# Kernel optimization log

Measured on AMD Instinct MI355X. Metric: run time of the kernel, lower is better.

The kernel has to match this reference:

```python
import jax, jax.numpy as jnp
import numpy as np

N_NODES = 50000


def _gcn_norm(edge_index, num_nodes):
    # Add self-loops (PyG GCNConv default) and compute symmetric norm.
    loops = jnp.arange(num_nodes, dtype=edge_index.dtype)
    src = jnp.concatenate([edge_index[0], loops])
    dst = jnp.concatenate([edge_index[1], loops])
    ones = jnp.ones(src.shape[0], dtype=jnp.float32)
    deg = jax.ops.segment_sum(ones, dst, num_segments=num_nodes)
    deg_inv_sqrt = jnp.where(deg > 0, jax.lax.rsqrt(jnp.maximum(deg, 1.0)), 0.0)
    norm = deg_inv_sqrt[src] * deg_inv_sqrt[dst]  # [E + N]
    return src, dst, norm


def _gcn_conv(x, src, dst, norm, W, b, num_nodes):
    xw = x @ W                               # [N, out]
    msg = xw[src] * norm[:, None]            # gather + scale  [E+N, out]
    out = jax.ops.segment_sum(msg, dst, num_segments=num_nodes)  # scatter-add
    return out + b


def setup_inputs() -> dict:
    key = jax.random.key(0)
    ks = jax.random.split(key, 10)
    d_in, d_h, d_out = 64, 64, 8
    n_edges = 800000
    x = jax.random.normal(ks[0], (N_NODES, d_in), dtype=jnp.float32)
    edge_index = jax.random.randint(ks[1], (2, n_edges), 0, N_NODES, dtype=jnp.int64)
    def w(k, fan_in, fan_out):
        return jax.random.normal(k, (fan_in, fan_out), dtype=jnp.float32) * (1.0 / np.sqrt(fan_in))
    return {
        "x": x,
        "edge_index": edge_index,
        "W0": w(ks[2], d_in, d_h), "b0": jnp.zeros((d_h,), jnp.float32),
        "W1": w(ks[3], d_h, d_h), "b1": jnp.zeros((d_h,), jnp.float32),
        "W2": w(ks[4], d_h, d_h), "b2": jnp.zeros((d_h,), jnp.float32),
        "linW": w(ks[5], d_h, d_out), "linb": jnp.zeros((d_out,), jnp.float32),
    }


def reference(x, edge_index, W0, b0, W1, b1, W2, b2, linW, linb):
    num_nodes = x.shape[0]
    src, dst, norm = _gcn_norm(edge_index, num_nodes)
    # 3 GCNConv layers, ReLU; dropout is identity at inference (training=False).
    for W, b in ((W0, b0), (W1, b1), (W2, b2)):
        x = jax.nn.relu(_gcn_conv(x, src, dst, norm, W, b, num_nodes))
    return x @ linW + linb
```

## Files before the change

### kernel.cpp

```cpp
#include <hip/hip_runtime.h>
#include <hip/hip_fp16.h>

#define TPB 256
#define CAP 8192
#define CAPSH 13


__device__ __forceinline__ int ld_idx(const void* p, long long i, int is64) {
    return is64 ? (int)((const long long*)p)[i] : ((const int*)p)[i];
}

__global__ void init_all(const unsigned int* w, int* flag, int* gcur) {
    int t = threadIdx.x;
    gcur[t] = t << CAPSH;
    if (t < 64) {
        unsigned int v = w[2 * t + 1];
        unsigned long long m = __ballot(v != 0u);
        if (t == 0) *flag = (m == 0ull) ? 1 : 0;
    }
}

__global__ __launch_bounds__(TPB) void p3_scatter(const void* ei, long long E,
                                                  const int* flag, int* gcur,
                                                  int* pairs) {
    __shared__ int cnt[TPB];
    __shared__ int cur2[TPB];
    int t = threadIdx.x;
    cnt[t] = 0;
    __syncthreads();
    int is64 = *flag;
    long long chunk = (E + gridDim.x - 1) / gridDim.x;
    long long s0 = (long long)blockIdx.x * chunk;
    long long s1 = (s0 + chunk < E) ? s0 + chunk : E;
    for (long long e = s0 + t; e < s1; e += TPB) {
        int d = ld_idx(ei, E + e, is64);
        atomicAdd(&cnt[d >> 8], 1);
    }
    __syncthreads();
    if (cnt[t]) cur2[t] = atomicAdd(&gcur[t], cnt[t]);
    __syncthreads();
    for (long long e = s0 + t; e < s1; e += TPB) {
        int sv = ld_idx(ei, e, is64);
        int d  = ld_idx(ei, E + e, is64);
        int pos = atomicAdd(&cur2[d >> 8], 1);
        pairs[pos] = (sv << 8) | (d & 255);
    }
}

__global__ __launch_bounds__(TPB) void p4_fill(const int* __restrict__ pairs,
                                               const int* __restrict__ gcur,
                                               int* __restrict__ deg,
                                               float* __restrict__ dis,
                                               int* __restrict__ offsets,
                                               int* __restrict__ csr, int n) {
    __shared__ int ldeg[TPB];
    __shared__ int s[TPB];
    __shared__ int cur[TPB];
    int t = threadIdx.x;
    int b = blockIdx.x;
    int base = b << CAPSH;
    int ecnt = gcur[b] - base;
    ldeg[t] = 0;
    __syncthreads();
    for (int e = base + t; e < base + ecnt; e += TPB)
        atomicAdd(&ldeg[pairs[e] & 255], 1);
    __syncthreads();
    int dv = ldeg[t];
    s[t] = dv;
    __syncthreads();
    for (int off = 1; off < TPB; off <<= 1) {
        int u = 0;
        if (t >= off) u = s[t - off];
        __syncthreads();
        s[t] += u;
        __syncthreads();
    }
    int o = base + s[t] - dv;
    cur[t] = o;
    int node = (b << 8) + t;
    if (node < n) {
        deg[node] = dv;
        dis[node] = rsqrtf((float)(dv + 1));
        offsets[node] = o;
    }
    __syncthreads();
    for (int e = base + t; e < base + ecnt; e += TPB) {
        int p = pairs[e];
        int pos = atomicAdd(&cur[p & 255], 1);
        csr[pos] = p >> 8;
    }
}

__device__ __forceinline__ float4 h4_to_f4(ushort4 v) {
    float4 r;
    r.x = __half2float(__ushort_as_half(v.x));
    r.y = __half2float(__ushort_as_half(v.y));
    r.z = __half2float(__ushort_as_half(v.z));
    r.w = __half2float(__ushort_as_half(v.w));
    return r;
}

__device__ __forceinline__ ushort4 f4_to_h4(float4 v) {
    ushort4 r;
    r.x = __half_as_ushort(__float2half_rn(v.x));
    r.y = __half_as_ushort(__float2half_rn(v.y));
    r.z = __half_as_ushort(__float2half_rn(v.z));
    r.w = __half_as_ushort(__float2half_rn(v.w));
    return r;
}

__device__ __forceinline__ float4 gather_rows(const ushort4* __restrict__ y4,
                                              const int* __restrict__ csr,
                                              int start, int cnt, int c,
                                              float4 acc) {
    const int base = threadIdx.x & 48;
    int j = 0;
    while (j + 16 <= cnt) {
        int idx = csr[start + j + c];
        #pragma unroll
        for (int k = 0; k < 16; ++k) {
            int s = __shfl(idx, base + k);
            float4 v = h4_to_f4(y4[s * 16 + c]);
            acc.x += v.x; acc.y += v.y; acc.z += v.z; acc.w += v.w;
        }
        j += 16;
    }
    int rem = cnt - j;
    if (rem > 0) {
        int idx = (c < rem) ? csr[start + j + c] : 0;
        #pragma unroll
        for (int k = 0; k < 15; ++k) {
            if (k < rem) {
                int s = __shfl(idx, base + k);
                float4 v = h4_to_f4(y4[s * 16 + c]);
                acc.x += v.x; acc.y += v.y; acc.z += v.z; acc.w += v.w;
            }
        }
    }
    return acc;
}

__global__ __launch_bounds__(TPB) void mm_first(const float* __restrict__ x,
                                                const float* __restrict__ W,
                                                const float* __restrict__ dis,
                                                ushort4* __restrict__ yout, int n) {
    __shared__ float Ws[64 * 64];
    __shared__ float hs[16][68];
    int t = threadIdx.x;
    const float4* W4g = (const float4*)W;
    float4* Ws4 = (float4*)Ws;
    #pragma unroll
    for (int i = 0; i < 4; ++i) Ws4[t + i * TPB] = W4g[t + i * TPB];

    int ni = t >> 4, c = t & 15;
    int node = blockIdx.x * 16 + ni;
    float4 h = {0.f, 0.f, 0.f, 0.f};
    float dv = 0.f;
    if (node < n) {
        h = ((const float4*)x)[node * 16 + c];
        dv = dis[node];
    }
    *(float4*)&hs[ni][c * 4] = h;
    __syncthreads();

    float4 o = {0.f, 0.f, 0.f, 0.f};
    #pragma unroll
    for (int k = 0; k < 64; ++k) {
        float hv = hs[ni][k];
        float4 w = Ws4[k * 16 + c];
        o.x = fmaf(hv, w.x, o.x);
        o.y = fmaf(hv, w.y, o.y);
        o.z = fmaf(hv, w.z, o.z);
        o.w = fmaf(hv, w.w, o.w);
    }
    if (node < n) {
        float4 r = {o.x * dv, o.y * dv, o.z * dv, o.w * dv};
        yout[node * 16 + c] = f4_to_h4(r);
    }
}

__global__ __launch_bounds__(TPB) void agg_mm(const ushort4* __restrict__ y,
                                              const int* __restrict__ csr,
                                              const int* __restrict__ offsets,
                                              const int* __restrict__ deg,
                                              const float* __restrict__ dis,
                                              const float* __restrict__ b,
                                              const float* __restrict__ W,
                                              ushort4* __restrict__ yout, int n) {
    __shared__ float Ws[64 * 64];
    __shared__ float hs[16][68];
    int t = threadIdx.x;
    const float4* W4g = (const float4*)W;
    float4* Ws4 = (float4*)Ws;
    #pragma unroll
    for (int i = 0; i < 4; ++i) Ws4[t + i * TPB] = W4g[t + i * TPB];

    int ni = t >> 4, c = t & 15;
    int node = blockIdx.x * 16 + ni;
    float4 h = {0.f, 0.f, 0.f, 0.f};
    float dv = 0.f;
    if (node < n) {
        float4 acc = h4_to_f4(y[node * 16 + c]);
        int start = offsets[node];
        int cnt = deg[node];
        acc = gather_rows(y, csr, start, cnt, c, acc);
        dv = dis[node];
        float4 bb = ((const float4*)b)[c];
        h.x = fmaxf(fmaf(dv, acc.x, bb.x), 0.f);
        h.y = fmaxf(fmaf(dv, acc.y, bb.y), 0.f);
        h.z = fmaxf(fmaf(dv, acc.z, bb.z), 0.f);
        h.w = fmaxf(fmaf(dv, acc.w, bb.w), 0.f);
    }
    *(float4*)&hs[ni][c * 4] = h;
    __syncthreads();

    float4 o = {0.f, 0.f, 0.f, 0.f};
    #pragma unroll
    for (int k = 0; k < 64; ++k) {
        float hv = hs[ni][k];
        float4 w = Ws4[k * 16 + c];
        o.x = fmaf(hv, w.x, o.x);
        o.y = fmaf(hv, w.y, o.y);
        o.z = fmaf(hv, w.z, o.z);
        o.w = fmaf(hv, w.w, o.w);
    }
    if (node < n) {
        float4 r = {o.x * dv, o.y * dv, o.z * dv, o.w * dv};
        yout[node * 16 + c] = f4_to_h4(r);
    }
}

__global__ __launch_bounds__(TPB) void agg_final(const ushort4* __restrict__ y,
                                                 const int* __restrict__ csr,
                                                 const int* __restrict__ offsets,
                                                 const int* __restrict__ deg,
                                                 const float* __restrict__ dis,
                                                 const float* __restrict__ b,
                                                 const float* __restrict__ Wl,
                                                 const float* __restrict__ bl,
                                                 float* __restrict__ out, int n) {
    __shared__ float Wls[64 * 8];
    __shared__ float bls[8];
    __shared__ float hs[16][68];
    int t = threadIdx.x;
    if (t < 128) ((float4*)Wls)[t] = ((const float4*)Wl)[t];
    if (t < 8) bls[t] = bl[t];

    int ni = t >> 4, c = t & 15;
    int node = blockIdx.x * 16 + ni;
    float4 h = {0.f, 0.f, 0.f, 0.f};
    if (node < n) {
        float4 acc = h4_to_f4(y[node * 16 + c]);
        int start = offsets[node];
        int cnt = deg[node];
        acc = gather_rows(y, csr, start, cnt, c, acc);
        float dv = dis[node];
        float4 bb = ((const float4*)b)[c];
        h.x = fmaxf(fmaf(dv, acc.x, bb.x), 0.f);
        h.y = fmaxf(fmaf(dv, acc.y, bb.y), 0.f);
        h.z = fmaxf(fmaf(dv, acc.z, bb.z), 0.f);
        h.w = fmaxf(fmaf(dv, acc.w, bb.w), 0.f);
    }
    *(float4*)&hs[ni][c * 4] = h;
    __syncthreads();

    if (c < 8 && node < n) {
        float acc = bls[c];
        #pragma unroll
        for (int k = 0; k < 64; ++k)
            acc = fmaf(hs[ni][k], Wls[k * 8 + c], acc);
        out[node * 8 + c] = acc;
    }
}

extern "C" void kernel_launch(void* const* d_in, const int* in_sizes, int n_in,
                              void* d_out, int out_size, void* d_ws, size_t ws_size,
                              hipStream_t stream) {
    const float* x  = (const float*)d_in[0];
    const void*  ei = d_in[1];
    const float* W[3]  = {(const float*)d_in[2], (const float*)d_in[4], (const float*)d_in[6]};
    const float* bv[3] = {(const float*)d_in[3], (const float*)d_in[5], (const float*)d_in[7]};
    const float* Wl = (const float*)d_in[8];
    const float* bl = (const float*)d_in[9];

    const long long E = in_sizes[1] / 2;
    const int dh = in_sizes[3];
    const int din = in_sizes[2] / dh;
    const int N = in_sizes[0] / din;
    const int nb = (N + 255) >> 8;

    char* ws = (char*)d_ws;
    size_t off = 0;
    auto alloc = [&](size_t bytes) -> char* {
        char* r = ws + off;
        off += (bytes + 255) & ~(size_t)255;
        return r;
    };
    int*     flag    = (int*)    alloc(4);
    int*     gcur    = (int*)    alloc(1024);
    int*     deg     = (int*)    alloc((size_t)N * 4);
    int*     offsets = (int*)    alloc((size_t)N * 4);
    float*   dis     = (float*)  alloc((size_t)N * 4);
    int*     pairs   = (int*)    alloc((size_t)nb * CAP * 4);
    int*     csr     = (int*)    alloc((size_t)nb * CAP * 4);
    ushort4* ybA     = (ushort4*)alloc((size_t)N * 64 * 2);
    ushort4* ybB     = (ushort4*)alloc((size_t)N * 64 * 2);

    init_all<<<1, TPB, 0, stream>>>((const unsigned int*)ei, flag, gcur);
    p3_scatter<<<256, TPB, 0, stream>>>(ei, E, flag, gcur, pairs);
    p4_fill<<<nb, TPB, 0, stream>>>(pairs, gcur, deg, dis, offsets, csr, N);

    const int gL = (N + 15) / 16;
    mm_first<<<gL, TPB, 0, stream>>>(x, W[0], dis, ybA, N);
    agg_mm<<<gL, TPB, 0, stream>>>(ybA, csr, offsets, deg, dis, bv[0], W[1], ybB, N);
    agg_mm<<<gL, TPB, 0, stream>>>(ybB, csr, offsets, deg, dis, bv[1], W[2], ybA, N);
    agg_final<<<gL, TPB, 0, stream>>>(ybA, csr, offsets, deg, dis, bv[2], Wl, bl,
                                      (float*)d_out, N);
}
```

Before: 224.2 us.

## Fuse all GCN stages into one persistent cooperative kernel with grid syncs

Replaces the seven separate launches (init, bucket scatter, CSR fill, first matmul, two aggregate+matmul layers, final aggregate+linear) with one cooperative kernel. Blocks loop over virtual blocks or node groups, and `grid.sync()` separates the stages. The aim is to remove per-launch gaps and tail effects between the small kernels. The price is grid-wide barrier cost, a grid capped by occupancy that may shrink parallelism per stage, and host-side occupancy and attribute queries on every call. It also relies on wave64 lockstep for the unsynchronised shared `hs` row reuse.

```diff
diff --git a/kernel.cpp b/kernel.cpp
--- a/kernel.cpp
+++ b/kernel.cpp
@@ -1,94 +1,16 @@
 #include <hip/hip_runtime.h>
 #include <hip/hip_fp16.h>
+#include <hip/hip_cooperative_groups.h>
+namespace cg = cooperative_groups;
 
 #define TPB 256
 #define CAP 8192
 #define CAPSH 13
+#define SCATTER_BLOCKS 256
 
 
 __device__ __forceinline__ int ld_idx(const void* p, long long i, int is64) {
     return is64 ? (int)((const long long*)p)[i] : ((const int*)p)[i];
-}
-
-__global__ void init_all(const unsigned int* w, int* flag, int* gcur) {
-    int t = threadIdx.x;
-    gcur[t] = t << CAPSH;
-    if (t < 64) {
-        unsigned int v = w[2 * t + 1];
-        unsigned long long m = __ballot(v != 0u);
-        if (t == 0) *flag = (m == 0ull) ? 1 : 0;
-    }
-}
-
-__global__ __launch_bounds__(TPB) void p3_scatter(const void* ei, long long E,
-                                                  const int* flag, int* gcur,
-                                                  int* pairs) {
-    __shared__ int cnt[TPB];
-    __shared__ int cur2[TPB];
-    int t = threadIdx.x;
-    cnt[t] = 0;
-    __syncthreads();
-    int is64 = *flag;
-    long long chunk = (E + gridDim.x - 1) / gridDim.x;
-    long long s0 = (long long)blockIdx.x * chunk;
-    long long s1 = (s0 + chunk < E) ? s0 + chunk : E;
-    for (long long e = s0 + t; e < s1; e += TPB) {
-        int d = ld_idx(ei, E + e, is64);
-        atomicAdd(&cnt[d >> 8], 1);
-    }
-    __syncthreads();
-    if (cnt[t]) cur2[t] = atomicAdd(&gcur[t], cnt[t]);
-    __syncthreads();
-    for (long long e = s0 + t; e < s1; e += TPB) {
-        int sv = ld_idx(ei, e, is64);
-        int d  = ld_idx(ei, E + e, is64);
-        int pos = atomicAdd(&cur2[d >> 8], 1);
-        pairs[pos] = (sv << 8) | (d & 255);
-    }
-}
-
-__global__ __launch_bounds__(TPB) void p4_fill(const int* __restrict__ pairs,
-                                               const int* __restrict__ gcur,
-                                               int* __restrict__ deg,
-                                               float* __restrict__ dis,
-                                               int* __restrict__ offsets,
-                                               int* __restrict__ csr, int n) {
-    __shared__ int ldeg[TPB];
-    __shared__ int s[TPB];
-    __shared__ int cur[TPB];
-    int t = threadIdx.x;
-    int b = blockIdx.x;
-    int base = b << CAPSH;
-    int ecnt = gcur[b] - base;
-    ldeg[t] = 0;
-    __syncthreads();
-    for (int e = base + t; e < base + ecnt; e += TPB)
-        atomicAdd(&ldeg[pairs[e] & 255], 1);
-    __syncthreads();
-    int dv = ldeg[t];
-    s[t] = dv;
-    __syncthreads();
-    for (int off = 1; off < TPB; off <<= 1) {
-        int u = 0;
-        if (t >= off) u = s[t - off];
-        __syncthreads();
-        s[t] += u;
-        __syncthreads();
-    }
-    int o = base + s[t] - dv;
-    cur[t] = o;
-    int node = (b << 8) + t;
-    if (node < n) {
-        deg[node] = dv;
-        dis[node] = rsqrtf((float)(dv + 1));
-        offsets[node] = o;
-    }
-    __syncthreads();
-    for (int e = base + t; e < base + ecnt; e += TPB) {
-        int p = pairs[e];
-        int pos = atomicAdd(&cur[p & 255], 1);
-        csr[pos] = p >> 8;
-    }
 }
 
 __device__ __forceinline__ float4 h4_to_f4(ushort4 v) {
@@ -140,136 +62,202 @@
     return acc;
 }
 
-__global__ __launch_bounds__(TPB) void mm_first(const float* __restrict__ x,
-                                                const float* __restrict__ W,
-                                                const float* __restrict__ dis,
-                                                ushort4* __restrict__ yout, int n) {
+__global__ __launch_bounds__(TPB, 4) void gcn_all(
+    const void* ei, long long E, int N, int nb, int nGroups,
+    const float* __restrict__ x,
+    const float* __restrict__ W0, const float* __restrict__ b0,
+    const float* __restrict__ W1, const float* __restrict__ b1,
+    const float* __restrict__ W2, const float* __restrict__ b2,
+    const float* __restrict__ Wl, const float* __restrict__ bl,
+    int* gcur, int* deg, float* dis, int* offsets,
+    int* pairs, int* csr,
+    ushort4* ybA, ushort4* ybB, float* out)
+{
+    cg::grid_group grid = cg::this_grid();
     __shared__ float Ws[64 * 64];
     __shared__ float hs[16][68];
-    int t = threadIdx.x;
-    const float4* W4g = (const float4*)W;
-    float4* Ws4 = (float4*)Ws;
-    #pragma unroll
-    for (int i = 0; i < 4; ++i) Ws4[t + i * TPB] = W4g[t + i * TPB];
-
-    int ni = t >> 4, c = t & 15;
-    int node = blockIdx.x * 16 + ni;
-    float4 h = {0.f, 0.f, 0.f, 0.f};
-    float dv = 0.f;
-    if (node < n) {
-        h = ((const float4*)x)[node * 16 + c];
-        dv = dis[node];
-    }
-    *(float4*)&hs[ni][c * 4] = h;
+    __shared__ int s_is64;
+    const int t = threadIdx.x;
+    const int ni = t >> 4, c = t & 15;
+
+    if (t < 64) {
+        const unsigned int* w = (const unsigned int*)ei;
+        unsigned long long m = __ballot(w[2 * t + 1] != 0u);
+        if (t == 0) s_is64 = (m == 0ull) ? 1 : 0;
+    }
+    if (blockIdx.x == 0) gcur[t] = t << CAPSH;
     __syncthreads();
-
-    float4 o = {0.f, 0.f, 0.f, 0.f};
-    #pragma unroll
-    for (int k = 0; k < 64; ++k) {
-        float hv = hs[ni][k];
-        float4 w = Ws4[k * 16 + c];
-        o.x = fmaf(hv, w.x, o.x);
-        o.y = fmaf(hv, w.y, o.y);
-        o.z = fmaf(hv, w.z, o.z);
-        o.w = fmaf(hv, w.w, o.w);
-    }
-    if (node < n) {
-        float4 r = {o.x * dv, o.y * dv, o.z * dv, o.w * dv};
-        yout[node * 16 + c] = f4_to_h4(r);
-    }
-}
-
-__global__ __launch_bounds__(TPB) void agg_mm(const ushort4* __restrict__ y,
-                                              const int* __restrict__ csr,
-                                              const int* __restrict__ offsets,
-                                              const int* __restrict__ deg,
-                                              const float* __restrict__ dis,
-                                              const float* __restrict__ b,
-                                              const float* __restrict__ W,
-                                              ushort4* __restrict__ yout, int n) {
-    __shared__ float Ws[64 * 64];
-    __shared__ float hs[16][68];
-    int t = threadIdx.x;
-    const float4* W4g = (const float4*)W;
-    float4* Ws4 = (float4*)Ws;
-    #pragma unroll
-    for (int i = 0; i < 4; ++i) Ws4[t + i * TPB] = W4g[t + i * TPB];
-
-    int ni = t >> 4, c = t & 15;
-    int node = blockIdx.x * 16 + ni;
-    float4 h = {0.f, 0.f, 0.f, 0.f};
-    float dv = 0.f;
-    if (node < n) {
-        float4 acc = h4_to_f4(y[node * 16 + c]);
-        int start = offsets[node];
-        int cnt = deg[node];
-        acc = gather_rows(y, csr, start, cnt, c, acc);
-        dv = dis[node];
-        float4 bb = ((const float4*)b)[c];
-        h.x = fmaxf(fmaf(dv, acc.x, bb.x), 0.f);
-        h.y = fmaxf(fmaf(dv, acc.y, bb.y), 0.f);
-        h.z = fmaxf(fmaf(dv, acc.z, bb.z), 0.f);
-        h.w = fmaxf(fmaf(dv, acc.w, bb.w), 0.f);
-    }
-    *(float4*)&hs[ni][c * 4] = h;
-    __syncthreads();
-
-    float4 o = {0.f, 0.f, 0.f, 0.f};
-    #pragma unroll
-    for (int k = 0; k < 64; ++k) {
-        float hv = hs[ni][k];
-        float4 w = Ws4[k * 16 + c];
-        o.x = fmaf(hv, w.x, o.x);
-        o.y = fmaf(hv, w.y, o.y);
-        o.z = fmaf(hv, w.z, o.z);
-        o.w = fmaf(hv, w.w, o.w);
-    }
-    if (node < n) {
-        float4 r = {o.x * dv, o.y * dv, o.z * dv, o.w * dv};
-        yout[node * 16 + c] = f4_to_h4(r);
-    }
-}
-
-__global__ __launch_bounds__(TPB) void agg_final(const ushort4* __restrict__ y,
-                                                 const int* __restrict__ csr,
-                                                 const int* __restrict__ offsets,
-                                                 const int* __restrict__ deg,
-                                                 const float* __restrict__ dis,
-                                                 const float* __restrict__ b,
-                                                 const float* __restrict__ Wl,
-                                                 const float* __restrict__ bl,
-                                                 float* __restrict__ out, int n) {
-    __shared__ float Wls[64 * 8];
-    __shared__ float bls[8];
-    __shared__ float hs[16][68];
-    int t = threadIdx.x;
-    if (t < 128) ((float4*)Wls)[t] = ((const float4*)Wl)[t];
-    if (t < 8) bls[t] = bl[t];
-
-    int ni = t >> 4, c = t & 15;
-    int node = blockIdx.x * 16 + ni;
-    float4 h = {0.f, 0.f, 0.f, 0.f};
-    if (node < n) {
-        float4 acc = h4_to_f4(y[node * 16 + c]);
-        int start = offsets[node];
-        int cnt = deg[node];
-        acc = gather_rows(y, csr, start, cnt, c, acc);
-        float dv = dis[node];
-        float4 bb = ((const float4*)b)[c];
-        h.x = fmaxf(fmaf(dv, acc.x, bb.x), 0.f);
-        h.y = fmaxf(fmaf(dv, acc.y, bb.y), 0.f);
-        h.z = fmaxf(fmaf(dv, acc.z, bb.z), 0.f);
-        h.w = fmaxf(fmaf(dv, acc.w, bb.w), 0.f);
-    }
-    *(float4*)&hs[ni][c * 4] = h;
-    __syncthreads();
-
-    if (c < 8 && node < n) {
-        float acc = bls[c];
+    const int is64 = s_is64;
+    grid.sync();
+
+    {
+        int* cnt  = (int*)Ws;
+        int* cur2 = cnt + 256;
+        long long chunk = (E + SCATTER_BLOCKS - 1) / SCATTER_BLOCKS;
+        for (int vb = blockIdx.x; vb < SCATTER_BLOCKS; vb += gridDim.x) {
+            cnt[t] = 0;
+            __syncthreads();
+            long long s0 = (long long)vb * chunk;
+            long long s1 = (s0 + chunk < E) ? s0 + chunk : E;
+            for (long long e = s0 + t; e < s1; e += TPB)
+                atomicAdd(&cnt[ld_idx(ei, E + e, is64) >> 8], 1);
+            __syncthreads();
+            if (cnt[t]) cur2[t] = atomicAdd(&gcur[t], cnt[t]);
+            __syncthreads();
+            for (long long e = s0 + t; e < s1; e += TPB) {
+                int sv = ld_idx(ei, e, is64);
+                int d  = ld_idx(ei, E + e, is64);
+                int pos = atomicAdd(&cur2[d >> 8], 1);
+                pairs[pos] = (sv << 8) | (d & 255);
+            }
+            __syncthreads();
+        }
+    }
+    grid.sync();
+
+    {
+        int* ldeg = (int*)Ws;
+        int* ssc  = ldeg + 256;
+        int* cur  = ssc + 256;
+        for (int b = blockIdx.x; b < nb; b += gridDim.x) {
+            int base = b << CAPSH;
+            int ecnt = gcur[b] - base;
+            ldeg[t] = 0;
+            __syncthreads();
+            for (int e = base + t; e < base + ecnt; e += TPB)
+                atomicAdd(&ldeg[pairs[e] & 255], 1);
+            __syncthreads();
+            int dv = ldeg[t];
+            ssc[t] = dv;
+            __syncthreads();
+            for (int off = 1; off < TPB; off <<= 1) {
+                int u = 0;
+                if (t >= off) u = ssc[t - off];
+                __syncthreads();
+                ssc[t] += u;
+                __syncthreads();
+            }
+            int o = base + ssc[t] - dv;
+            cur[t] = o;
+            int node = (b << 8) + t;
+            if (node < N) {
+                deg[node] = dv;
+                dis[node] = rsqrtf((float)(dv + 1));
+                offsets[node] = o;
+            }
+            __syncthreads();
+            for (int e = base + t; e < base + ecnt; e += TPB) {
+                int p = pairs[e];
+                int pos = atomicAdd(&cur[p & 255], 1);
+                csr[pos] = p >> 8;
+            }
+            __syncthreads();
+        }
+    }
+    grid.sync();
+
+    {
+        float4* Ws4 = (float4*)Ws;
+        const float4* W4g = (const float4*)W0;
         #pragma unroll
-        for (int k = 0; k < 64; ++k)
-            acc = fmaf(hs[ni][k], Wls[k * 8 + c], acc);
-        out[node * 8 + c] = acc;
+        for (int i = 0; i < 4; ++i) Ws4[t + i * TPB] = W4g[t + i * TPB];
+        __syncthreads();
+        for (int g = blockIdx.x; g < nGroups; g += gridDim.x) {
+            int node = g * 16 + ni;
+            float4 h = {0.f, 0.f, 0.f, 0.f};
+            float dv = 0.f;
+            if (node < N) {
+                h = ((const float4*)x)[node * 16 + c];
+                dv = dis[node];
+            }
+            *(float4*)&hs[ni][c * 4] = h;
+            float4 o = {0.f, 0.f, 0.f, 0.f};
+            #pragma unroll
+            for (int k = 0; k < 64; ++k) {
+                float hv = hs[ni][k];
+                float4 w = Ws4[k * 16 + c];
+                o.x = fmaf(hv, w.x, o.x);
+                o.y = fmaf(hv, w.y, o.y);
+                o.z = fmaf(hv, w.z, o.z);
+                o.w = fmaf(hv, w.w, o.w);
+            }
+            if (node < N) {
+                float4 r = {o.x * dv, o.y * dv, o.z * dv, o.w * dv};
+                ybA[node * 16 + c] = f4_to_h4(r);
+            }
+        }
+    }
+    grid.sync();
+
+    for (int L = 0; L < 2; ++L) {
+        const ushort4* yin  = (L == 0) ? ybA : ybB;
+        ushort4*       yout = (L == 0) ? ybB : ybA;
+        const float*   Wv   = (L == 0) ? W1 : W2;
+        const float*   bvec = (L == 0) ? b0 : b1;
+        float4* Ws4 = (float4*)Ws;
+        const float4* W4g = (const float4*)Wv;
+        #pragma unroll
+        for (int i = 0; i < 4; ++i) Ws4[t + i * TPB] = W4g[t + i * TPB];
+        __syncthreads();
+        for (int g = blockIdx.x; g < nGroups; g += gridDim.x) {
+            int node = g * 16 + ni;
+            float4 h = {0.f, 0.f, 0.f, 0.f};
+            float dv = 0.f;
+            if (node < N) {
+                float4 acc = h4_to_f4(yin[node * 16 + c]);
+                acc = gather_rows(yin, csr, offsets[node], deg[node], c, acc);
+                dv = dis[node];
+                float4 bb = ((const float4*)bvec)[c];
+                h.x = fmaxf(fmaf(dv, acc.x, bb.x), 0.f);
+                h.y = fmaxf(fmaf(dv, acc.y, bb.y), 0.f);
+                h.z = fmaxf(fmaf(dv, acc.z, bb.z), 0.f);
+                h.w = fmaxf(fmaf(dv, acc.w, bb.w), 0.f);
+            }
+            *(float4*)&hs[ni][c * 4] = h;
+            float4 o = {0.f, 0.f, 0.f, 0.f};
+            #pragma unroll
+            for (int k = 0; k < 64; ++k) {
+                float hv = hs[ni][k];
+                float4 w = Ws4[k * 16 + c];
+                o.x = fmaf(hv, w.x, o.x);
+                o.y = fmaf(hv, w.y, o.y);
+                o.z = fmaf(hv, w.z, o.z);
+                o.w = fmaf(hv, w.w, o.w);
+            }
+            if (node < N) {
+                float4 r = {o.x * dv, o.y * dv, o.z * dv, o.w * dv};
+                yout[node * 16 + c] = f4_to_h4(r);
+            }
+        }
+        grid.sync();
+    }
+
+    {
+        if (t < 128) ((float4*)Ws)[t] = ((const float4*)Wl)[t];
+        if (t < 8)  Ws[512 + t] = bl[t];
+        __syncthreads();
+        for (int g = blockIdx.x; g < nGroups; g += gridDim.x) {
+            int node = g * 16 + ni;
+            float4 h = {0.f, 0.f, 0.f, 0.f};
+            if (node < N) {
+                float4 acc = h4_to_f4(ybA[node * 16 + c]);
+                acc = gather_rows(ybA, csr, offsets[node], deg[node], c, acc);
+                float dv = dis[node];
+                float4 bb = ((const float4*)b2)[c];
+                h.x = fmaxf(fmaf(dv, acc.x, bb.x), 0.f);
+                h.y = fmaxf(fmaf(dv, acc.y, bb.y), 0.f);
+                h.z = fmaxf(fmaf(dv, acc.z, bb.z), 0.f);
+                h.w = fmaxf(fmaf(dv, acc.w, bb.w), 0.f);
+            }
+            *(float4*)&hs[ni][c * 4] = h;
+            if (c < 8 && node < N) {
+                float acc = Ws[512 + c];
+                #pragma unroll
+                for (int k = 0; k < 64; ++k)
+                    acc = fmaf(hs[ni][k], Ws[k * 8 + c], acc);
+                out[node * 8 + c] = acc;
+            }
+        }
     }
 }
 
@@ -278,16 +266,21 @@
                               hipStream_t stream) {
     const float* x  = (const float*)d_in[0];
     const void*  ei = d_in[1];
-    const float* W[3]  = {(const float*)d_in[2], (const float*)d_in[4], (const float*)d_in[6]};
-    const float* bv[3] = {(const float*)d_in[3], (const float*)d_in[5], (const float*)d_in[7]};
+    const float* W0 = (const float*)d_in[2];
+    const float* b0 = (const float*)d_in[3];
+    const float* W1 = (const float*)d_in[4];
+    const float* b1 = (const float*)d_in[5];
+    const float* W2 = (const float*)d_in[6];
+    const float* b2 = (const float*)d_in[7];
     const float* Wl = (const float*)d_in[8];
     const float* bl = (const float*)d_in[9];
 
-    const long long E = in_sizes[1] / 2;
+    long long E = in_sizes[1] / 2;
     const int dh = in_sizes[3];
     const int din = in_sizes[2] / dh;
-    const int N = in_sizes[0] / din;
-    const int nb = (N + 255) >> 8;
+    int N = in_sizes[0] / din;
+    int nb = (N + 255) >> 8;
+    int nGroups = (N + 15) / 16;
 
     char* ws = (char*)d_ws;
     size_t off = 0;
@@ -296,7 +289,6 @@
         off += (bytes + 255) & ~(size_t)255;
         return r;
     };
-    int*     flag    = (int*)    alloc(4);
     int*     gcur    = (int*)    alloc(1024);
     int*     deg     = (int*)    alloc((size_t)N * 4);
     int*     offsets = (int*)    alloc((size_t)N * 4);
@@ -305,15 +297,24 @@
     int*     csr     = (int*)    alloc((size_t)nb * CAP * 4);
     ushort4* ybA     = (ushort4*)alloc((size_t)N * 64 * 2);
     ushort4* ybB     = (ushort4*)alloc((size_t)N * 64 * 2);
-
-    init_all<<<1, TPB, 0, stream>>>((const unsigned int*)ei, flag, gcur);
-    p3_scatter<<<256, TPB, 0, stream>>>(ei, E, flag, gcur, pairs);
-    p4_fill<<<nb, TPB, 0, stream>>>(pairs, gcur, deg, dis, offsets, csr, N);
-
-    const int gL = (N + 15) / 16;
-    mm_first<<<gL, TPB, 0, stream>>>(x, W[0], dis, ybA, N);
-    agg_mm<<<gL, TPB, 0, stream>>>(ybA, csr, offsets, deg, dis, bv[0], W[1], ybB, N);
-    agg_mm<<<gL, TPB, 0, stream>>>(ybB, csr, offsets, deg, dis, bv[1], W[2], ybA, N);
-    agg_final<<<gL, TPB, 0, stream>>>(ybA, csr, offsets, deg, dis, bv[2], Wl, bl,
-                                      (float*)d_out, N);
-}
+    float*   outp    = (float*)d_out;
+
+    int occ = 0, numCU = 256;
+    hipOccupancyMaxActiveBlocksPerMultiprocessor(&occ, (const void*)gcn_all,
+                                                 TPB, 0);
+    hipDeviceGetAttribute(&numCU, hipDeviceAttributeMultiprocessorCount, 0);
+    if (occ < 1) occ = 1;
+    long long g = (long long)occ * numCU;
+    int grid = (g > 1024) ? 1024 : (int)g;
+
+    void* args[] = {
+        (void*)&ei, (void*)&E, (void*)&N, (void*)&nb, (void*)&nGroups,
+        (void*)&x,
+        (void*)&W0, (void*)&b0, (void*)&W1, (void*)&b1,
+        (void*)&W2, (void*)&b2, (void*)&Wl, (void*)&bl,
+        (void*)&gcur, (void*)&deg, (void*)&dis, (void*)&offsets,
+        (void*)&pairs, (void*)&csr, (void*)&ybA, (void*)&ybB, (void*)&outp
+    };
+    hipLaunchCooperativeKernel((const void*)gcn_all, dim3(grid), dim3(TPB),
+                               args, 0, stream);
+}
```

Measured after the change: 634.9 us. +183.2%, slower.

## Fuse CSR fill with first-layer matmul and pack per-node metadata into int2

Applied to the files above, without the earlier changes.

The CSR-building kernel now also computes the first layer's x@W0 scaled by the degree norm for its 256 nodes, removing a separate kernel launch. The degree norm comes from shared memory instead of a global dis array. Per-node offset, degree and rsqrt-degree are packed into one int2, so the aggregation kernels make a single load instead of three. In exchange, the first matmul runs on only about 200 blocks, each looping over 16 groups of nodes, which lowers parallelism for that step. The packing also assumes degree below 1024 and offsets that fit in 22 bits.

```diff
diff --git a/kernel.cpp b/kernel.cpp
--- a/kernel.cpp
+++ b/kernel.cpp
@@ -47,50 +47,6 @@
     }
 }
 
-__global__ __launch_bounds__(TPB) void p4_fill(const int* __restrict__ pairs,
-                                               const int* __restrict__ gcur,
-                                               int* __restrict__ deg,
-                                               float* __restrict__ dis,
-                                               int* __restrict__ offsets,
-                                               int* __restrict__ csr, int n) {
-    __shared__ int ldeg[TPB];
-    __shared__ int s[TPB];
-    __shared__ int cur[TPB];
-    int t = threadIdx.x;
-    int b = blockIdx.x;
-    int base = b << CAPSH;
-    int ecnt = gcur[b] - base;
-    ldeg[t] = 0;
-    __syncthreads();
-    for (int e = base + t; e < base + ecnt; e += TPB)
-        atomicAdd(&ldeg[pairs[e] & 255], 1);
-    __syncthreads();
-    int dv = ldeg[t];
-    s[t] = dv;
-    __syncthreads();
-    for (int off = 1; off < TPB; off <<= 1) {
-        int u = 0;
-        if (t >= off) u = s[t - off];
-        __syncthreads();
-        s[t] += u;
-        __syncthreads();
-    }
-    int o = base + s[t] - dv;
-    cur[t] = o;
-    int node = (b << 8) + t;
-    if (node < n) {
-        deg[node] = dv;
-        dis[node] = rsqrtf((float)(dv + 1));
-        offsets[node] = o;
-    }
-    __syncthreads();
-    for (int e = base + t; e < base + ecnt; e += TPB) {
-        int p = pairs[e];
-        int pos = atomicAdd(&cur[p & 255], 1);
-        csr[pos] = p >> 8;
-    }
-}
-
 __device__ __forceinline__ float4 h4_to_f4(ushort4 v) {
     float4 r;
     r.x = __half2float(__ushort_as_half(v.x));
@@ -107,6 +63,83 @@
     r.z = __half_as_ushort(__float2half_rn(v.z));
     r.w = __half_as_ushort(__float2half_rn(v.w));
     return r;
+}
+
+__global__ __launch_bounds__(TPB) void p4_fill_mm(const int* __restrict__ pairs,
+                                                  const int* __restrict__ gcur,
+                                                  const float* __restrict__ x,
+                                                  const float* __restrict__ W0,
+                                                  int2* __restrict__ meta,
+                                                  int* __restrict__ csr,
+                                                  ushort4* __restrict__ ybA,
+                                                  int N) {
+    __shared__ float Ws[64 * 64];
+    __shared__ float hs[16][68];
+    __shared__ float fdis[256];
+    int* ldeg = (int*)Ws;
+    int* ssc  = ldeg + 256;
+    int* cur  = ssc + 256;
+    int t = threadIdx.x;
+    int b = blockIdx.x;
+    int base = b << CAPSH;
+    int ecnt = gcur[b] - base;
+    ldeg[t] = 0;
+    __syncthreads();
+    for (int e = base + t; e < base + ecnt; e += TPB)
+        atomicAdd(&ldeg[pairs[e] & 255], 1);
+    __syncthreads();
+    int dv = ldeg[t];
+    ssc[t] = dv;
+    __syncthreads();
+    for (int off = 1; off < TPB; off <<= 1) {
+        int u = 0;
+        if (t >= off) u = ssc[t - off];
+        __syncthreads();
+        ssc[t] += u;
+        __syncthreads();
+    }
+    int o = base + ssc[t] - dv;
+    cur[t] = o;
+    float dd = rsqrtf((float)(dv + 1));
+    fdis[t] = dd;
+    int node = (b << 8) + t;
+    if (node < N)
+        meta[node] = make_int2((o << 10) | dv, __float_as_int(dd));
+    __syncthreads();
+    for (int e = base + t; e < base + ecnt; e += TPB) {
+        int p = pairs[e];
+        int pos = atomicAdd(&cur[p & 255], 1);
+        csr[pos] = p >> 8;
+    }
+    __syncthreads();
+
+    float4* Ws4 = (float4*)Ws;
+    const float4* W4g = (const float4*)W0;
+    #pragma unroll
+    for (int i = 0; i < 4; ++i) Ws4[t + i * TPB] = W4g[t + i * TPB];
+    __syncthreads();
+    int ni = t >> 4, c = t & 15;
+    for (int p = 0; p < 16; ++p) {
+        int nd = (b << 8) + p * 16 + ni;
+        float4 h = {0.f, 0.f, 0.f, 0.f};
+        if (nd < N) h = ((const float4*)x)[nd * 16 + c];
+        *(float4*)&hs[ni][c * 4] = h;
+        float4 oacc = {0.f, 0.f, 0.f, 0.f};
+        #pragma unroll
+        for (int k = 0; k < 64; ++k) {
+            float hv = hs[ni][k];
+            float4 w = Ws4[k * 16 + c];
+            oacc.x = fmaf(hv, w.x, oacc.x);
+            oacc.y = fmaf(hv, w.y, oacc.y);
+            oacc.z = fmaf(hv, w.z, oacc.z);
+            oacc.w = fmaf(hv, w.w, oacc.w);
+        }
+        if (nd < N) {
+            float dvv = fdis[p * 16 + ni];
+            float4 r = {oacc.x * dvv, oacc.y * dvv, oacc.z * dvv, oacc.w * dvv};
+            ybA[nd * 16 + c] = f4_to_h4(r);
+        }
+    }
 }
 
 __device__ __forceinline__ float4 gather_rows(const ushort4* __restrict__ y4,
@@ -140,10 +173,12 @@
     return acc;
 }
 
-__global__ __launch_bounds__(TPB) void mm_first(const float* __restrict__ x,
-                                                const float* __restrict__ W,
-                                                const float* __restrict__ dis,
-                                                ushort4* __restrict__ yout, int n) {
+__global__ __launch_bounds__(TPB) void agg_mm(const ushort4* __restrict__ y,
+                                              const int* __restrict__ csr,
+                                              const int2* __restrict__ meta,
+                                              const float* __restrict__ b,
+                                              const float* __restrict__ W,
+                                              ushort4* __restrict__ yout, int n) {
     __shared__ float Ws[64 * 64];
     __shared__ float hs[16][68];
     int t = threadIdx.x;
@@ -157,12 +192,20 @@
     float4 h = {0.f, 0.f, 0.f, 0.f};
     float dv = 0.f;
     if (node < n) {
-        h = ((const float4*)x)[node * 16 + c];
-        dv = dis[node];
-    }
+        int2 m = meta[node];
+        int start = ((unsigned)m.x) >> 10;
+        int cnt = m.x & 1023;
+        dv = __int_as_float(m.y);
+        float4 acc = h4_to_f4(y[node * 16 + c]);
+        acc = gather_rows(y, csr, start, cnt, c, acc);
+        float4 bb = ((const float4*)b)[c];
+        h.x = fmaxf(fmaf(dv, acc.x, bb.x), 0.f);
+        h.y = fmaxf(fmaf(dv, acc.y, bb.y), 0.f);
+        h.z = fmaxf(fmaf(dv, acc.z, bb.z), 0.f);
+        h.w = fmaxf(fmaf(dv, acc.w, bb.w), 0.f);
+    }
+    __syncthreads();
     *(float4*)&hs[ni][c * 4] = h;
-    __syncthreads();
-
     float4 o = {0.f, 0.f, 0.f, 0.f};
     #pragma unroll
     for (int k = 0; k < 64; ++k) {
@@ -179,62 +222,9 @@
     }
 }
 
-__global__ __launch_bounds__(TPB) void agg_mm(const ushort4* __restrict__ y,
-                                              const int* __restrict__ csr,
-                                              const int* __restrict__ offsets,
-                                              const int* __restrict__ deg,
-                                              const float* __restrict__ dis,
-                                              const float* __restrict__ b,
-                                              const float* __restrict__ W,
-                                              ushort4* __restrict__ yout, int n) {
-    __shared__ float Ws[64 * 64];
-    __shared__ float hs[16][68];
-    int t = threadIdx.x;
-    const float4* W4g = (const float4*)W;
-    float4* Ws4 = (float4*)Ws;
-    #pragma unroll
-    for (int i = 0; i < 4; ++i) Ws4[t + i * TPB] = W4g[t + i * TPB];
-
-    int ni = t >> 4, c = t & 15;
-    int node = blockIdx.x * 16 + ni;
-    float4 h = {0.f, 0.f, 0.f, 0.f};
-    float dv = 0.f;
-    if (node < n) {
-        float4 acc = h4_to_f4(y[node * 16 + c]);
-        int start = offsets[node];
-        int cnt = deg[node];
-        acc = gather_rows(y, csr, start, cnt, c, acc);
-        dv = dis[node];
-        float4 bb = ((const float4*)b)[c];
-        h.x = fmaxf(fmaf(dv, acc.x, bb.x), 0.f);
-        h.y = fmaxf(fmaf(dv, acc.y, bb.y), 0.f);
-        h.z = fmaxf(fmaf(dv, acc.z, bb.z), 0.f);
-        h.w = fmaxf(fmaf(dv, acc.w, bb.w), 0.f);
-    }
-    *(float4*)&hs[ni][c * 4] = h;
-    __syncthreads();
-
-    float4 o = {0.f, 0.f, 0.f, 0.f};
-    #pragma unroll
-    for (int k = 0; k < 64; ++k) {
-        float hv = hs[ni][k];
-        float4 w = Ws4[k * 16 + c];
-        o.x = fmaf(hv, w.x, o.x);
-        o.y = fmaf(hv, w.y, o.y);
-        o.z = fmaf(hv, w.z, o.z);
-        o.w = fmaf(hv, w.w, o.w);
-    }
-    if (node < n) {
-        float4 r = {o.x * dv, o.y * dv, o.z * dv, o.w * dv};
-        yout[node * 16 + c] = f4_to_h4(r);
-    }
-}
-
 __global__ __launch_bounds__(TPB) void agg_final(const ushort4* __restrict__ y,
                                                  const int* __restrict__ csr,
-                                                 const int* __restrict__ offsets,
-                                                 const int* __restrict__ deg,
-                                                 const float* __restrict__ dis,
+                                                 const int2* __restrict__ meta,
                                                  const float* __restrict__ b,
                                                  const float* __restrict__ Wl,
                                                  const float* __restrict__ bl,
@@ -250,20 +240,20 @@
     int node = blockIdx.x * 16 + ni;
     float4 h = {0.f, 0.f, 0.f, 0.f};
     if (node < n) {
+        int2 m = meta[node];
+        int start = ((unsigned)m.x) >> 10;
+        int cnt = m.x & 1023;
+        float dv = __int_as_float(m.y);
         float4 acc = h4_to_f4(y[node * 16 + c]);
-        int start = offsets[node];
-        int cnt = deg[node];
         acc = gather_rows(y, csr, start, cnt, c, acc);
-        float dv = dis[node];
         float4 bb = ((const float4*)b)[c];
         h.x = fmaxf(fmaf(dv, acc.x, bb.x), 0.f);
         h.y = fmaxf(fmaf(dv, acc.y, bb.y), 0.f);
         h.z = fmaxf(fmaf(dv, acc.z, bb.z), 0.f);
         h.w = fmaxf(fmaf(dv, acc.w, bb.w), 0.f);
     }
+    __syncthreads();
     *(float4*)&hs[ni][c * 4] = h;
-    __syncthreads();
-
     if (c < 8 && node < n) {
         float acc = bls[c];
         #pragma unroll
@@ -278,8 +268,12 @@
                               hipStream_t stream) {
     const float* x  = (const float*)d_in[0];
     const void*  ei = d_in[1];
-    const float* W[3]  = {(const float*)d_in[2], (const float*)d_in[4], (const float*)d_in[6]};
-    const float* bv[3] = {(const float*)d_in[3], (const float*)d_in[5], (const float*)d_in[7]};
+    const float* W0 = (const float*)d_in[2];
+    const float* b0 = (const float*)d_in[3];
+    const float* W1 = (const float*)d_in[4];
+    const float* b1 = (const float*)d_in[5];
+    const float* W2 = (const float*)d_in[6];
+    const float* b2 = (const float*)d_in[7];
     const float* Wl = (const float*)d_in[8];
     const float* bl = (const float*)d_in[9];
 
@@ -298,9 +292,7 @@
     };
     int*     flag    = (int*)    alloc(4);
     int*     gcur    = (int*)    alloc(1024);
-    int*     deg     = (int*)    alloc((size_t)N * 4);
-    int*     offsets = (int*)    alloc((size_t)N * 4);
-    float*   dis     = (float*)  alloc((size_t)N * 4);
+    int2*    meta    = (int2*)   alloc((size_t)N * 8);
     int*     pairs   = (int*)    alloc((size_t)nb * CAP * 4);
     int*     csr     = (int*)    alloc((size_t)nb * CAP * 4);
     ushort4* ybA     = (ushort4*)alloc((size_t)N * 64 * 2);
@@ -308,12 +300,11 @@
 
     init_all<<<1, TPB, 0, stream>>>((const unsigned int*)ei, flag, gcur);
     p3_scatter<<<256, TPB, 0, stream>>>(ei, E, flag, gcur, pairs);
-    p4_fill<<<nb, TPB, 0, stream>>>(pairs, gcur, deg, dis, offsets, csr, N);
+    p4_fill_mm<<<nb, TPB, 0, stream>>>(pairs, gcur, x, W0, meta, csr, ybA, N);
 
     const int gL = (N + 15) / 16;
-    mm_first<<<gL, TPB, 0, stream>>>(x, W[0], dis, ybA, N);
-    agg_mm<<<gL, TPB, 0, stream>>>(ybA, csr, offsets, deg, dis, bv[0], W[1], ybB, N);
-    agg_mm<<<gL, TPB, 0, stream>>>(ybB, csr, offsets, deg, dis, bv[1], W[2], ybA, N);
-    agg_final<<<gL, TPB, 0, stream>>>(ybA, csr, offsets, deg, dis, bv[2], Wl, bl,
+    agg_mm<<<gL, TPB, 0, stream>>>(ybA, csr, meta, b0, W1, ybB, N);
+    agg_mm<<<gL, TPB, 0, stream>>>(ybB, csr, meta, b1, W2, ybA, N);
+    agg_final<<<gL, TPB, 0, stream>>>(ybA, csr, meta, b2, Wl, bl,
                                       (float*)d_out, N);
 }
```

Measured after the change: 238.5 us. 6.4% more time.
